# Performance work log

Hardware: AMD Instinct MI355X
Metric: run time of the kernel (lower is better)

## Reference

```python
import jax, jax.numpy as jnp
import numpy as np

MID = 64      # mid_channels
KSQ = 9       # kernel_size**2

def setup_inputs() -> dict:
    key = jax.random.key(0)
    k1, k2 = jax.random.split(key, 2)
    x = jax.random.normal(k1, (8, 256, 128, 128), dtype=jnp.float32)
    # 1x1 conv weight [out_c=640, in_c=256]; fan-in scaled init like torch Conv2d
    W = jax.random.normal(k2, (MID * (1 + KSQ), 256), dtype=jnp.float32) * (1.0 / np.sqrt(256.0))
    b = jnp.zeros((MID * (1 + KSQ),), dtype=jnp.float32)
    return {"x": x, "W": W, "b": b}

def reference(x, W, b):
    B, C, H, Wd = x.shape
    # 1x1 conv == channel contraction
    raw = jnp.einsum('bchw,oc->bohw', x, W) + b[None, :, None, None]   # [B, 640, H, W]
    score_map = raw[:, :MID]                                           # [B, MID, H, W]
    kernel_map = raw[:, MID:].reshape(B, MID, KSQ, H, Wd)              # [B, MID, 9, H, W]
    # adaptive_avg_pool2d(.,1) -> mean over HW, then sigmoid
    global_scores = jax.nn.sigmoid(score_map.mean(axis=(2, 3)))        # [B, MID]
    norm_kernels = jax.nn.softmax(kernel_map, axis=2)                  # softmax over 9-tap kernel dim
    # eval mode: scale from current global scores, clamped
    scale = jnp.clip(global_scores.mean(), 0.25, 1.0)
    k = int(np.ceil(MID * float(scale)))
    k = max(k, max(4, MID // 4))
    # topk channel selection per sample
    _, idx_full = jax.lax.top_k(global_scores, MID)
    indices = idx_full[:, :k]                                          # [B, k]
    # scatter ones into mask
    mask = jnp.zeros_like(global_scores).at[jnp.arange(B)[:, None], indices].set(1.0)
    mask = mask[:, :, None, None]                                      # [B, MID, 1, 1]
    return (mask, norm_kernels, k, indices)
```

## Files before the change

kernel.cpp:

```cpp
#include <hip/hip_runtime.h>
#include <math.h>

constexpr int CIN      = 256;
constexpr int HW       = 16384;
constexpr int NMID     = 64;
constexpr int HWTILE   = 128;
constexpr int TILE_B   = 8192;
constexpr int NORM_OFF = 512;
constexpr int K_OFF    = 75497984;
constexpr int IDX_OFF  = 75497985;

typedef __attribute__((ext_vector_type(8))) short bf16x8;
typedef __attribute__((ext_vector_type(4))) float f32x4;

__device__ __forceinline__ unsigned bf16_rne(float f) {
    unsigned u = __float_as_uint(f);
    return (u + 0x7fffu + ((u >> 16) & 1u)) >> 16;
}

__device__ __forceinline__ void gload_lds16(const void* gsrc, void* ldst) {
    __builtin_amdgcn_global_load_lds(
        (const __attribute__((address_space(1))) void*)gsrc,
        (__attribute__((address_space(3))) void*)ldst, 16, 0, 0);
}

__global__ __launch_bounds__(256) void prep_w(const float* __restrict__ Wm,
                                              char* __restrict__ ws)
{
    const int o = blockIdx.x;
    const int c = threadIdx.x;
    int mid, j;
    if (o < NMID) { mid = o; j = 0; }
    else          { mid = (o - NMID) / 9; j = 1 + (o - NMID) % 9; }
    const int g  = mid >> 3, ml = mid & 7, q = ml >> 1, mi = ml & 1;
    const int idx = mi * 10 + j;
    const int p   = (idx >> 2) * 16 + q * 4 + (idx & 3);
    const float w = Wm[(size_t)o * CIN + c];
    const unsigned hi = bf16_rne(w);
    const float    fl = w - __uint_as_float(hi << 16);
    const unsigned lo = bf16_rne(fl);
    const int kc = c >> 5, cc = c & 31;
    char* base = ws + (size_t)((g * 8 + kc) * 2) * TILE_B + p * 80 + cc * 2;
    *(unsigned short*)(base)          = (unsigned short)hi;
    *(unsigned short*)(base + TILE_B) = (unsigned short)lo;
}

__global__ __launch_bounds__(512) void zero_mask_kernel(float* __restrict__ out) {
    out[threadIdx.x] = 0.0f;
}

__global__ __launch_bounds__(256, 2) void fused_main(const float* __restrict__ x,
                                                     const char* __restrict__ wimg,
                                                     const float* __restrict__ bvec,
                                                     float* __restrict__ out)
{
    __shared__ __align__(16) char atile[3][2][TILE_B];
    __shared__ float bsh[576];

    const int tid  = threadIdx.x;
    const int wave = tid >> 6, lane = tid & 63;
    const int q    = lane >> 4, m = lane & 15;
    const int b    = blockIdx.x >> 7;
    const int hw0  = (blockIdx.x & 127) * HWTILE;
    const int grot = (blockIdx.x >> 3) & 7;

#define STAGE(tile, buf) do {                                                  \
    const char* _s = wimg + (size_t)(tile) * 2 * TILE_B;                       \
    char* _d = &atile[buf][0][0];                                              \
    gload_lds16(_s + tid * 16,                 _d + tid * 16);                 \
    gload_lds16(_s + 4096 + tid * 16,          _d + 4096 + tid * 16);          \
    gload_lds16(_s + TILE_B + tid * 16,        _d + TILE_B + tid * 16);        \
    gload_lds16(_s + TILE_B + 4096 + tid * 16, _d + TILE_B + 4096 + tid * 16); \
} while (0)

    const int t0 = grot * 8;
    STAGE(t0, 0);
    STAGE(t0 + 1, 1);

    bf16x8 Bhi[2][8], Blo[2][8];
    const float* xb = x + (size_t)b * CIN * HW + hw0 + wave * 32 + m;
    #pragma unroll
    for (int t = 0; t < 2; ++t)
        #pragma unroll
        for (int kc = 0; kc < 8; ++kc) {
            float f[8];
            #pragma unroll
            for (int i = 0; i < 8; ++i)
                f[i] = xb[t * 16 + (size_t)(kc * 32 + q * 8 + i) * HW];
            union { unsigned u[4]; bf16x8 v; } uh, ul;
            #pragma unroll
            for (int jj = 0; jj < 4; ++jj) {
                const unsigned h0 = bf16_rne(f[2*jj]), h1 = bf16_rne(f[2*jj+1]);
                const float r0 = f[2*jj]   - __uint_as_float(h0 << 16);
                const float r1 = f[2*jj+1] - __uint_as_float(h1 << 16);
                uh.u[jj] = h0 | (h1 << 16);
                ul.u[jj] = bf16_rne(r0) | (bf16_rne(r1) << 16);
            }
            Bhi[t][kc] = uh.v; Blo[t][kc] = ul.v;
        }
    for (int i = tid; i < 576; i += 256) bsh[i] = bvec[NMID + i];
    asm volatile("s_waitcnt lgkmcnt(0)" ::: "memory");
    __builtin_amdgcn_s_barrier();

    int cur = 0;
    #pragma unroll 1
    for (int gg = 0; gg < 8; ++gg) {
        const int g = (gg + grot) & 7;
        f32x4 acc[5][2];
        #pragma unroll
        for (int ot = 0; ot < 5; ++ot)
            #pragma unroll
            for (int t = 0; t < 2; ++t) acc[ot][t] = (f32x4){0.f, 0.f, 0.f, 0.f};

        #pragma unroll
        for (int kc = 0; kc < 8; ++kc) {
            const int seq = gg * 8 + kc;
            const int nb  = (cur >= 1) ? cur - 1 : 2;
            if (seq <= 61) {
                const int nseq = seq + 2;
                STAGE((((nseq >> 3) + grot) & 7) * 8 + (nseq & 7), nb);
            }
            if (gg == 7 && kc == 7)      asm volatile("s_waitcnt vmcnt(0)"  ::: "memory");
            else if (gg == 7 && kc == 6) asm volatile("s_waitcnt vmcnt(4)"  ::: "memory");
            else if (gg > 0 && kc < 2)   asm volatile("s_waitcnt vmcnt(46)" ::: "memory");
            else                         asm volatile("s_waitcnt vmcnt(8)"  ::: "memory");
            __builtin_amdgcn_s_barrier();

            const char* ahi = &atile[cur][0][m * 80 + q * 16];
            const char* alo = &atile[cur][1][m * 80 + q * 16];
            bf16x8 Ah[5], Al[5];
            #pragma unroll
            for (int ot = 0; ot < 5; ++ot) {
                Ah[ot] = *(const bf16x8*)(ahi + ot * 1280);
                Al[ot] = *(const bf16x8*)(alo + ot * 1280);
            }
            __builtin_amdgcn_s_setprio(1);
            #pragma unroll
            for (int ot = 0; ot < 5; ++ot)
                #pragma unroll
                for (int t2 = 0; t2 < 2; ++t2)
                    acc[ot][t2] = __builtin_amdgcn_mfma_f32_16x16x32_bf16(Ah[ot], Bhi[t2][kc], acc[ot][t2], 0, 0, 0);
            #pragma unroll
            for (int ot = 0; ot < 5; ++ot)
                #pragma unroll
                for (int t2 = 0; t2 < 2; ++t2)
                    acc[ot][t2] = __builtin_amdgcn_mfma_f32_16x16x32_bf16(Ah[ot], Blo[t2][kc], acc[ot][t2], 0, 0, 0);
            #pragma unroll
            for (int ot = 0; ot < 5; ++ot)
                #pragma unroll
                for (int t2 = 0; t2 < 2; ++t2)
                    acc[ot][t2] = __builtin_amdgcn_mfma_f32_16x16x32_bf16(Al[ot], Bhi[t2][kc], acc[ot][t2], 0, 0, 0);
            __builtin_amdgcn_s_setprio(0);

            if (kc == 7) {
                #pragma unroll
                for (int mi = 0; mi < 2; ++mi) {
                    const int gmid = g * 8 + q * 2 + mi;
                    const int i0 = mi * 10;
                    float s = acc[i0 >> 2][0][i0 & 3] + acc[i0 >> 2][1][i0 & 3];
                    s += __shfl_xor(s, 1); s += __shfl_xor(s, 2);
                    s += __shfl_xor(s, 4); s += __shfl_xor(s, 8);
                    if (m == 0) atomicAdd(&out[b * NMID + gmid], s);
                    float bj[9];
                    #pragma unroll
                    for (int jj = 0; jj < 9; ++jj) bj[jj] = bsh[gmid * 9 + jj];
                    #pragma unroll
                    for (int t2 = 0; t2 < 2; ++t2) {
                        float p[9];
                        #pragma unroll
                        for (int jj = 0; jj < 9; ++jj) {
                            const int idx = i0 + 1 + jj;
                            p[jj] = acc[idx >> 2][t2][idx & 3] + bj[jj];
                        }
                        float mx = p[0];
                        #pragma unroll
                        for (int jj = 1; jj < 9; ++jj) mx = fmaxf(mx, p[jj]);
                        float ss = 0.f;
                        #pragma unroll
                        for (int jj = 0; jj < 9; ++jj) { p[jj] = __expf(p[jj] - mx); ss += p[jj]; }
                        const float rs = 1.0f / ss;
                        float* ob = out + NORM_OFF
                                  + ((size_t)((b * NMID + gmid) * 9)) * HW
                                  + hw0 + wave * 32 + t2 * 16 + m;
                        #pragma unroll
                        for (int jj = 0; jj < 9; ++jj)
                            __builtin_nontemporal_store(p[jj] * rs, ob + (size_t)jj * HW);
                    }
                }
            }
            asm volatile("s_waitcnt lgkmcnt(0)" ::: "memory");
            __builtin_amdgcn_s_barrier();
            cur = (cur == 2) ? 0 : cur + 1;
        }
    }
#undef STAGE
}

__global__ __launch_bounds__(512) void finalize_kernel(float* __restrict__ out,
                                                       const float* __restrict__ bvec,
                                                       int k)
{
    const int tid  = threadIdx.x;
    const int b    = tid >> 6;
    const int lane = tid & 63;
    const float sum = out[b * NMID + lane];
    const float sv  = 1.0f / (1.0f + __expf(-(sum * (1.0f / 16384.0f) + bvec[lane])));
    float val      = sv;
    float selected = 0.0f;
    for (int t = 0; t < k; ++t) {
        float bvv = val;
        int   bi  = lane;
        #pragma unroll
        for (int off = 32; off >= 1; off >>= 1) {
            const float ov = __shfl_xor(bvv, off);
            const int   oi = __shfl_xor(bi, off);
            if (ov > bvv || (ov == bvv && oi < bi)) { bvv = ov; bi = oi; }
        }
        if (lane == bi) { val = -INFINITY; selected = 1.0f; }
        if (lane == 0) out[IDX_OFF + b * k + t] = (float)bi;
    }
    out[b * NMID + lane] = selected;
    if (tid == 0) out[K_OFF] = (float)k;
}

extern "C" void kernel_launch(void* const* d_in, const int* in_sizes, int n_in,
                              void* d_out, int out_size, void* d_ws, size_t ws_size,
                              hipStream_t stream)
{
    const float* x    = (const float*)d_in[0];
    const float* Wm   = (const float*)d_in[1];
    const float* bvec = (const float*)d_in[2];
    float* out = (float*)d_out;
    char*  ws  = (char*)d_ws;

    const int k = (out_size - IDX_OFF) / 8;

    prep_w<<<640, 256, 0, stream>>>(Wm, ws);
    zero_mask_kernel<<<1, 512, 0, stream>>>(out);
    fused_main<<<8 * (HW / HWTILE), 256, 0, stream>>>(x, ws, bvec, out);
    finalize_kernel<<<1, 512, 0, stream>>>(out, bvec, k);
}
```

Before: 181.9 us.

## Drop split-bf16 emulation, use single bf16 GEMM and exact fp32 score path

```diff
diff --git a/kernel.cpp b/kernel.cpp
--- a/kernel.cpp
+++ b/kernel.cpp
@@ -9,6 +9,7 @@
 constexpr int NORM_OFF = 512;
 constexpr int K_OFF    = 75497984;
 constexpr int IDX_OFF  = 75497985;
+constexpr int XBAR_OFF = 64 * TILE_B;
 
 typedef __attribute__((ext_vector_type(8))) short bf16x8;
 typedef __attribute__((ext_vector_type(4))) float f32x4;
@@ -35,26 +36,24 @@
     const int g  = mid >> 3, ml = mid & 7, q = ml >> 1, mi = ml & 1;
     const int idx = mi * 10 + j;
     const int p   = (idx >> 2) * 16 + q * 4 + (idx & 3);
-    const float w = Wm[(size_t)o * CIN + c];
-    const unsigned hi = bf16_rne(w);
-    const float    fl = w - __uint_as_float(hi << 16);
-    const unsigned lo = bf16_rne(fl);
+    const unsigned hi = bf16_rne(Wm[(size_t)o * CIN + c]);
     const int kc = c >> 5, cc = c & 31;
-    char* base = ws + (size_t)((g * 8 + kc) * 2) * TILE_B + p * 80 + cc * 2;
-    *(unsigned short*)(base)          = (unsigned short)hi;
-    *(unsigned short*)(base + TILE_B) = (unsigned short)lo;
-}
-
-__global__ __launch_bounds__(512) void zero_mask_kernel(float* __restrict__ out) {
-    out[threadIdx.x] = 0.0f;
-}
-
-__global__ __launch_bounds__(256, 2) void fused_main(const float* __restrict__ x,
+    *(unsigned short*)(ws + (size_t)(g * 8 + kc) * TILE_B + p * 80 + cc * 2)
+        = (unsigned short)hi;
+}
+
+__global__ __launch_bounds__(512) void zero_xbar_kernel(float* __restrict__ xbar) {
+    #pragma unroll
+    for (int i = 0; i < 4; ++i) xbar[i * 512 + threadIdx.x] = 0.0f;
+}
+
+__global__ __launch_bounds__(256, 3) void fused_main(const float* __restrict__ x,
                                                      const char* __restrict__ wimg,
                                                      const float* __restrict__ bvec,
-                                                     float* __restrict__ out)
-{
-    __shared__ __align__(16) char atile[3][2][TILE_B];
+                                                     float* __restrict__ out,
+                                                     float* __restrict__ xbar)
+{
+    __shared__ __align__(16) char atile[3][TILE_B];
     __shared__ float bsh[576];
 
     const int tid  = threadIdx.x;
@@ -65,39 +64,50 @@
     const int grot = (blockIdx.x >> 3) & 7;
 
 #define STAGE(tile, buf) do {                                                  \
-    const char* _s = wimg + (size_t)(tile) * 2 * TILE_B;                       \
-    char* _d = &atile[buf][0][0];                                              \
-    gload_lds16(_s + tid * 16,                 _d + tid * 16);                 \
-    gload_lds16(_s + 4096 + tid * 16,          _d + 4096 + tid * 16);          \
-    gload_lds16(_s + TILE_B + tid * 16,        _d + TILE_B + tid * 16);        \
-    gload_lds16(_s + TILE_B + 4096 + tid * 16, _d + TILE_B + 4096 + tid * 16); \
+    const char* _s = wimg + (size_t)(tile) * TILE_B;                           \
+    char* _d = &atile[buf][0];                                                 \
+    gload_lds16(_s + tid * 16,        _d + tid * 16);                          \
+    gload_lds16(_s + 4096 + tid * 16, _d + 4096 + tid * 16);                   \
 } while (0)
 
     const int t0 = grot * 8;
     STAGE(t0, 0);
     STAGE(t0 + 1, 1);
 
-    bf16x8 Bhi[2][8], Blo[2][8];
+    bf16x8 Bhi[2][8];
     const float* xb = x + (size_t)b * CIN * HW + hw0 + wave * 32 + m;
     #pragma unroll
-    for (int t = 0; t < 2; ++t)
-        #pragma unroll
-        for (int kc = 0; kc < 8; ++kc) {
+    for (int kc = 0; kc < 8; ++kc) {
+        float xacc[8];
+        #pragma unroll
+        for (int i = 0; i < 8; ++i) xacc[i] = 0.0f;
+        #pragma unroll
+        for (int t = 0; t < 2; ++t) {
             float f[8];
             #pragma unroll
+            for (int i = 0; i < 8; ++i) {
+                f[i] = xb[t * 16 + (size_t)(kc * 32 + q * 8 + i) * HW];
+                xacc[i] += f[i];
+            }
+            union { unsigned u[4]; bf16x8 v; } uh;
+            #pragma unroll
+            for (int jj = 0; jj < 4; ++jj)
+                uh.u[jj] = bf16_rne(f[2*jj]) | (bf16_rne(f[2*jj+1]) << 16);
+            Bhi[t][kc] = uh.v;
+        }
+        #pragma unroll
+        for (int i = 0; i < 8; ++i) {
+            xacc[i] += __shfl_xor(xacc[i], 1);
+            xacc[i] += __shfl_xor(xacc[i], 2);
+            xacc[i] += __shfl_xor(xacc[i], 4);
+            xacc[i] += __shfl_xor(xacc[i], 8);
+        }
+        if (m == 0) {
+            #pragma unroll
             for (int i = 0; i < 8; ++i)
-                f[i] = xb[t * 16 + (size_t)(kc * 32 + q * 8 + i) * HW];
-            union { unsigned u[4]; bf16x8 v; } uh, ul;
-            #pragma unroll
-            for (int jj = 0; jj < 4; ++jj) {
-                const unsigned h0 = bf16_rne(f[2*jj]), h1 = bf16_rne(f[2*jj+1]);
-                const float r0 = f[2*jj]   - __uint_as_float(h0 << 16);
-                const float r1 = f[2*jj+1] - __uint_as_float(h1 << 16);
-                uh.u[jj] = h0 | (h1 << 16);
-                ul.u[jj] = bf16_rne(r0) | (bf16_rne(r1) << 16);
-            }
-            Bhi[t][kc] = uh.v; Blo[t][kc] = ul.v;
-        }
+                atomicAdd(&xbar[b * CIN + kc * 32 + q * 8 + i], xacc[i]);
+        }
+    }
     for (int i = tid; i < 576; i += 256) bsh[i] = bvec[NMID + i];
     asm volatile("s_waitcnt lgkmcnt(0)" ::: "memory");
     __builtin_amdgcn_s_barrier();
@@ -121,35 +131,22 @@
                 STAGE((((nseq >> 3) + grot) & 7) * 8 + (nseq & 7), nb);
             }
             if (gg == 7 && kc == 7)      asm volatile("s_waitcnt vmcnt(0)"  ::: "memory");
-            else if (gg == 7 && kc == 6) asm volatile("s_waitcnt vmcnt(4)"  ::: "memory");
-            else if (gg > 0 && kc < 2)   asm volatile("s_waitcnt vmcnt(46)" ::: "memory");
-            else                         asm volatile("s_waitcnt vmcnt(8)"  ::: "memory");
+            else if (gg == 7 && kc == 6) asm volatile("s_waitcnt vmcnt(2)"  ::: "memory");
+            else if (gg > 0 && kc < 2)   asm volatile("s_waitcnt vmcnt(40)" ::: "memory");
+            else                         asm volatile("s_waitcnt vmcnt(4)"  ::: "memory");
             __builtin_amdgcn_s_barrier();
 
-            const char* ahi = &atile[cur][0][m * 80 + q * 16];
-            const char* alo = &atile[cur][1][m * 80 + q * 16];
-            bf16x8 Ah[5], Al[5];
-            #pragma unroll
-            for (int ot = 0; ot < 5; ++ot) {
-                Ah[ot] = *(const bf16x8*)(ahi + ot * 1280);
-                Al[ot] = *(const bf16x8*)(alo + ot * 1280);
-            }
+            const char* ah = &atile[cur][m * 80 + q * 16];
+            bf16x8 Ah[5];
+            #pragma unroll
+            for (int ot = 0; ot < 5; ++ot)
+                Ah[ot] = *(const bf16x8*)(ah + ot * 1280);
             __builtin_amdgcn_s_setprio(1);
             #pragma unroll
             for (int ot = 0; ot < 5; ++ot)
                 #pragma unroll
                 for (int t2 = 0; t2 < 2; ++t2)
                     acc[ot][t2] = __builtin_amdgcn_mfma_f32_16x16x32_bf16(Ah[ot], Bhi[t2][kc], acc[ot][t2], 0, 0, 0);
-            #pragma unroll
-            for (int ot = 0; ot < 5; ++ot)
-                #pragma unroll
-                for (int t2 = 0; t2 < 2; ++t2)
-                    acc[ot][t2] = __builtin_amdgcn_mfma_f32_16x16x32_bf16(Ah[ot], Blo[t2][kc], acc[ot][t2], 0, 0, 0);
-            #pragma unroll
-            for (int ot = 0; ot < 5; ++ot)
-                #pragma unroll
-                for (int t2 = 0; t2 < 2; ++t2)
-                    acc[ot][t2] = __builtin_amdgcn_mfma_f32_16x16x32_bf16(Al[ot], Bhi[t2][kc], acc[ot][t2], 0, 0, 0);
             __builtin_amdgcn_s_setprio(0);
 
             if (kc == 7) {
@@ -157,10 +154,6 @@
                 for (int mi = 0; mi < 2; ++mi) {
                     const int gmid = g * 8 + q * 2 + mi;
                     const int i0 = mi * 10;
-                    float s = acc[i0 >> 2][0][i0 & 3] + acc[i0 >> 2][1][i0 & 3];
-                    s += __shfl_xor(s, 1); s += __shfl_xor(s, 2);
-                    s += __shfl_xor(s, 4); s += __shfl_xor(s, 8);
-                    if (m == 0) atomicAdd(&out[b * NMID + gmid], s);
                     float bj[9];
                     #pragma unroll
                     for (int jj = 0; jj < 9; ++jj) bj[jj] = bsh[gmid * 9 + jj];
@@ -197,14 +190,23 @@
 }
 
 __global__ __launch_bounds__(512) void finalize_kernel(float* __restrict__ out,
+                                                       const float* __restrict__ Wm,
                                                        const float* __restrict__ bvec,
+                                                       const float* __restrict__ xbar,
                                                        int k)
 {
     const int tid  = threadIdx.x;
     const int b    = tid >> 6;
     const int lane = tid & 63;
-    const float sum = out[b * NMID + lane];
-    const float sv  = 1.0f / (1.0f + __expf(-(sum * (1.0f / 16384.0f) + bvec[lane])));
+    const float4* wr = (const float4*)(Wm + (size_t)lane * CIN);
+    const float4* xr = (const float4*)(xbar + b * CIN);
+    float dot = 0.f;
+    #pragma unroll 8
+    for (int c4 = 0; c4 < CIN / 4; ++c4) {
+        const float4 w = wr[c4], xv = xr[c4];
+        dot += w.x * xv.x + w.y * xv.y + w.z * xv.z + w.w * xv.w;
+    }
+    const float sv = 1.0f / (1.0f + __expf(-(dot * (1.0f / 16384.0f) + bvec[lane])));
     float val      = sv;
     float selected = 0.0f;
     for (int t = 0; t < k; ++t) {
@@ -230,13 +232,14 @@
     const float* x    = (const float*)d_in[0];
     const float* Wm   = (const float*)d_in[1];
     const float* bvec = (const float*)d_in[2];
-    float* out = (float*)d_out;
-    char*  ws  = (char*)d_ws;
+    float* out  = (float*)d_out;
+    char*  ws   = (char*)d_ws;
+    float* xbar = (float*)(ws + XBAR_OFF);
 
     const int k = (out_size - IDX_OFF) / 8;
 
     prep_w<<<640, 256, 0, stream>>>(Wm, ws);
-    zero_mask_kernel<<<1, 512, 0, stream>>>(out);
-    fused_main<<<8 * (HW / HWTILE), 256, 0, stream>>>(x, ws, bvec, out);
-    finalize_kernel<<<1, 512, 0, stream>>>(out, bvec, k);
-}
+    zero_xbar_kernel<<<1, 512, 0, stream>>>(xbar);
+    fused_main<<<8 * (HW / HWTILE), 256, 0, stream>>>(x, ws, bvec, out, xbar);
+    finalize_kernel<<<1, 512, 0, stream>>>(out, Wm, bvec, xbar, k);
+}
```

Result: slower. 447.4 us (+146.0%).
